# Kernel tuning notes

Hardware: AMD Instinct MI355X
Metric: run time of the kernel (lower is better)

The kernel has to match this reference:

```python
import jax, jax.numpy as jnp
import numpy as np

B, L, DIM = 4, 2048, 1024
EXPAND, D_STATE, D_CONV = 2, 16, 4
D_INNER = EXPAND * DIM          # 2048
DT_RANK = DIM // 16             # 64
MLP_HID = 4 * DIM


def setup_inputs() -> dict:
    key = jax.random.key(0)
    ks = jax.random.split(key, 20)
    s = 0.02
    inp = {
        "hidden_states": jax.random.normal(ks[0], (B, L, DIM), jnp.float32),
        "cond": jax.random.normal(ks[1], (B, DIM), jnp.float32),
        # norm (LayerNorm with affine)
        "norm_w": jnp.ones((DIM,), jnp.float32),
        "norm_b": jnp.zeros((DIM,), jnp.float32),
        # adaLN: Linear(dim, 6*dim)
        "ada_w": jax.random.normal(ks[2], (6 * DIM, DIM), jnp.float32) * s,
        "ada_b": jnp.zeros((6 * DIM,), jnp.float32),
        # Mamba mixer params
        "in_proj_w": jax.random.normal(ks[3], (2 * D_INNER, DIM), jnp.float32) * s,
        "conv_w": jax.random.normal(ks[4], (D_INNER, 1, D_CONV), jnp.float32) * s,
        "conv_b": jnp.zeros((D_INNER,), jnp.float32),
        "x_proj_w": jax.random.normal(ks[5], (DT_RANK + 2 * D_STATE, D_INNER), jnp.float32) * s,
        "dt_proj_w": jax.random.normal(ks[6], (D_INNER, DT_RANK), jnp.float32) * s,
        "dt_proj_b": jax.random.uniform(ks[7], (D_INNER,), jnp.float32, -4.0, -2.0),
        "A_log": jnp.log(jnp.broadcast_to(jnp.arange(1, D_STATE + 1, dtype=jnp.float32), (D_INNER, D_STATE))),
        "Dp": jnp.ones((D_INNER,), jnp.float32),
        "out_proj_w": jax.random.normal(ks[8], (DIM, D_INNER), jnp.float32) * s,
        # MLP
        "fc1_w": jax.random.normal(ks[9], (MLP_HID, DIM), jnp.float32) * s,
        "fc1_b": jnp.zeros((MLP_HID,), jnp.float32),
        "fc2_w": jax.random.normal(ks[10], (DIM, MLP_HID), jnp.float32) * s,
        "fc2_b": jnp.zeros((DIM,), jnp.float32),
    }
    return inp


def _layernorm(x, w, b, eps):
    mu = jnp.mean(x, axis=-1, keepdims=True)
    var = jnp.mean(jnp.square(x - mu), axis=-1, keepdims=True)
    y = (x - mu) * jax.lax.rsqrt(var + eps)
    return y * w + b if w is not None else y


def _modulate(x, shift, scale):
    # x: [B,L,D]; shift/scale: [B,D]
    return x * (1.0 + scale[:, None, :]) + shift[:, None, :]


def _mamba(x_in, in_proj_w, conv_w, conv_b, x_proj_w, dt_proj_w, dt_proj_b, A_log, Dp, out_proj_w):
    # x_in: [B,L,DIM]
    xz = jnp.einsum("bld,ed->ble", x_in, in_proj_w)        # [B,L,2*Di]
    x, z = jnp.split(xz, 2, axis=-1)                        # each [B,L,Di]
    # causal depthwise conv over L
    x_ncl = jnp.transpose(x, (0, 2, 1))                     # [B,Di,L]
    x_ncl = jax.lax.conv_general_dilated(
        x_ncl, conv_w, window_strides=(1,), padding=[(D_CONV - 1, 0)],
        feature_group_count=D_INNER, dimension_numbers=("NCH", "OIH", "NCH"))
    x = jnp.transpose(x_ncl, (0, 2, 1)) + conv_b            # [B,L,Di]
    x = jax.nn.silu(x)
    x_dbl = jnp.einsum("bld,ed->ble", x, x_proj_w)          # [B,L,dt_rank+2*N]
    dt, Bm, Cm = jnp.split(x_dbl, [DT_RANK, DT_RANK + D_STATE], axis=-1)
    dt = jax.nn.softplus(jnp.einsum("blr,dr->bld", dt, dt_proj_w) + dt_proj_b)  # [B,L,Di]
    A = -jnp.exp(A_log)                                     # [Di,N]

    def step(h, inps):
        dt_t, B_t, C_t, x_t = inps                          # [B,Di],[B,N],[B,N],[B,Di]
        dA = jnp.exp(dt_t[..., None] * A)                   # [B,Di,N]
        dBx = (dt_t * x_t)[..., None] * B_t[:, None, :]     # [B,Di,N]
        h = h * dA + dBx
        y = jnp.einsum("bdn,bn->bd", h, C_t)
        return h, y

    h0 = jnp.zeros((x.shape[0], D_INNER, D_STATE), x.dtype)
    xs = (jnp.transpose(dt, (1, 0, 2)), jnp.transpose(Bm, (1, 0, 2)),
          jnp.transpose(Cm, (1, 0, 2)), jnp.transpose(x, (1, 0, 2)))
    _, ys = jax.lax.scan(step, h0, xs)                      # [L,B,Di]
    y = jnp.transpose(ys, (1, 0, 2)) + x * Dp               # [B,L,Di]
    y = y * jax.nn.silu(z)
    return jnp.einsum("bld,od->blo", y, out_proj_w)         # [B,L,DIM]


def reference(hidden_states, cond, norm_w, norm_b, ada_w, ada_b, in_proj_w, conv_w,
              conv_b, x_proj_w, dt_proj_w, dt_proj_b, A_log, Dp, out_proj_w,
              fc1_w, fc1_b, fc2_w, fc2_b):
    residual = hidden_states                                # residual=None path
    hs = _layernorm(residual, norm_w, norm_b, 1e-5)
    mods = jax.nn.silu(cond) @ ada_w.T + ada_b              # [B,6*DIM]
    shift_msa, scale_msa, gate_msa, shift_mlp, scale_mlp, gate_mlp = jnp.split(mods, 6, axis=1)
    hs = gate_msa[:, None, :] * _mamba(_modulate(hs, shift_msa, scale_msa),
                                       in_proj_w, conv_w, conv_b, x_proj_w,
                                       dt_proj_w, dt_proj_b, A_log, Dp, out_proj_w)
    h2 = _modulate(_layernorm(hs, None, None, 1e-6), shift_mlp, scale_mlp)
    h2 = jax.nn.gelu(h2 @ fc1_w.T + fc1_b, approximate=True) @ fc2_w.T + fc2_b
    hs = hs + gate_mlp[:, None, :] * h2
    return (hs, residual)
```

## Files before the change

### kernel.cpp

```cpp
#include <hip/hip_runtime.h>
#include <hip/hip_bf16.h>


typedef unsigned short ushort_t;
typedef __attribute__((ext_vector_type(8))) short short8;
typedef __attribute__((ext_vector_type(4))) float floatx4;
typedef __attribute__((ext_vector_type(4))) unsigned short ushort4v;

#define DEVI __device__ __forceinline__

DEVI float b2f(ushort_t u) { union { unsigned int i; float f; } v; v.i = ((unsigned int)u) << 16; return v.f; }
DEVI ushort_t f2b(float f) {
    union { float f; unsigned int i; } v; v.f = f;
    unsigned int r = v.i + 0x7fffu + ((v.i >> 16) & 1u);
    return (ushort_t)(r >> 16);
}
DEVI bool is_f32(const void* nw) { return ((const unsigned int*)nw)[0] == 0x3F800000u; }
DEVI float sigmoidf_(float x) { return 1.f / (1.f + __expf(-x)); }
DEVI float siluf_(float x) { return x * sigmoidf_(x); }
DEVI float softplusf_(float x) { return (x > 20.f) ? x : log1pf(__expf(x)); }
DEVI float gelu_tanh_(float x) {
    float c = 0.7978845608028654f * (x + 0.044715f * x * x * x);
    return 0.5f * x * (1.f + tanhf(c));
}
DEVI void async16(ushort_t* lds, const ushort_t* g) {
    __builtin_amdgcn_global_load_lds((const __attribute__((address_space(1))) void*)g,
                                     (__attribute__((address_space(3))) void*)lds,
                                     16, 0, 0);
}

DEVI void remap_tile(int bid, int Mt, int Nt, int& mt, int& nt) {
    const int nwg = Mt * Nt;
    const int cpx = nwg >> 3;
    const int v = (bid & 7) * cpx + (bid >> 3);
    if (((Mt & 7) == 0) && ((Nt & 7) == 0)) {
        const int s = v >> 6, w = v & 63;
        const int smt = s % (Mt >> 3), snt = s / (Mt >> 3);
        mt = smt * 8 + (w >> 3);
        nt = snt * 8 + (w & 7);
    } else {
        mt = v % Mt;
        nt = v / Mt;
    }
}

__global__ __launch_bounds__(256) void convert_all_kernel(
    const void* __restrict__ in_proj, const void* __restrict__ x_proj,
    const void* __restrict__ dt_w, const void* __restrict__ out_proj,
    const void* __restrict__ fc1_w, const void* __restrict__ fc2_w,
    const void* __restrict__ dt_b, const void* __restrict__ fc1_b,
    const void* __restrict__ fc2_b,
    ushort_t* __restrict__ w_in, ushort_t* __restrict__ w_xp,
    ushort_t* __restrict__ w_dt, ushort_t* __restrict__ w_out,
    ushort_t* __restrict__ w_fc1, ushort_t* __restrict__ w_fc2,
    float* __restrict__ dtb_f, float* __restrict__ fc1b_f,
    float* __restrict__ fc2b_f, const void* __restrict__ nw)
{
    const bool f32 = is_f32(nw);
    int b = blockIdx.x;
    const void* src; ushort_t* dst; int n8;
    if (b < 2048)      { src = in_proj;  dst = w_in;  n8 = 524288; }
    else if (b < 2144) { src = x_proj;   dst = w_xp;  n8 = 24576;  b -= 2048; }
    else if (b < 2208) { src = dt_w;     dst = w_dt;  n8 = 16384;  b -= 2144; }
    else if (b < 3232) { src = out_proj; dst = w_out; n8 = 262144; b -= 2208; }
    else if (b < 5280) { src = fc1_w;    dst = w_fc1; n8 = 524288; b -= 3232; }
    else if (b < 7328) { src = fc2_w;    dst = w_fc2; n8 = 524288; b -= 5280; }
    else {
        b -= 7328;
        const void* bs; float* bd; int n;
        if (b < 8)       { bs = dt_b;  bd = dtb_f;  n = 2048; }
        else if (b < 24) { bs = fc1_b; bd = fc1b_f; n = 4096; b -= 8; }
        else             { bs = fc2_b; bd = fc2b_f; n = 1024; b -= 24; }
        int i = b * 256 + threadIdx.x;
        if (i < n) bd[i] = f32 ? ((const float*)bs)[i] : b2f(((const ushort_t*)bs)[i]);
        return;
    }
    int i = b * 256 + threadIdx.x;
    if (i >= n8) return;
    if (f32) {
        const float4* s = (const float4*)src;
        float4 a = s[2 * i], c = s[2 * i + 1];
        short8 o;
        o[0] = (short)f2b(a.x); o[1] = (short)f2b(a.y);
        o[2] = (short)f2b(a.z); o[3] = (short)f2b(a.w);
        o[4] = (short)f2b(c.x); o[5] = (short)f2b(c.y);
        o[6] = (short)f2b(c.z); o[7] = (short)f2b(c.w);
        ((short8*)dst)[i] = o;
    } else {
        ((short8*)dst)[i] = ((const short8*)src)[i];
    }
}

__global__ __launch_bounds__(256) void ada_kernel(
    const void* __restrict__ condv, const void* __restrict__ ada_wv,
    const void* __restrict__ ada_bv, float* __restrict__ mods,
    const void* __restrict__ nw)
{
    __shared__ float sc[4096];
    const int tid = threadIdx.x;
    const bool f32 = is_f32(nw);
    if (f32) {
        const float* cf = (const float*)condv;
        for (int i = tid; i < 4096; i += 256) sc[i] = siluf_(cf[i]);
    } else {
        const ushort_t* cb = (const ushort_t*)condv;
        for (int i = tid; i < 4096; i += 256) sc[i] = siluf_(b2f(cb[i]));
    }
    __syncthreads();
    const int j = blockIdx.x * 256 + tid;
    float bb = f32 ? ((const float*)ada_bv)[j] : b2f(((const ushort_t*)ada_bv)[j]);
    float s0 = bb, s1 = bb, s2 = bb, s3 = bb;
    if (f32) {
        const float4* w4 = ((const float4*)ada_wv) + (size_t)j * 256;
        for (int d4 = 0; d4 < 256; d4++) {
            float4 w = w4[d4];
            float wv[4] = {w.x, w.y, w.z, w.w};
#pragma unroll
            for (int e = 0; e < 4; e++) {
                int d = d4 * 4 + e;
                s0 += sc[d] * wv[e];
                s1 += sc[1024 + d] * wv[e];
                s2 += sc[2048 + d] * wv[e];
                s3 += sc[3072 + d] * wv[e];
            }
        }
    } else {
        const ushort_t* wrow = ((const ushort_t*)ada_wv) + (size_t)j * 1024;
        for (int d = 0; d < 1024; d += 8) {
            short8 w8 = *(const short8*)(wrow + d);
#pragma unroll
            for (int e = 0; e < 8; e++) {
                float wv = b2f(((const ushort_t*)&w8)[e]);
                s0 += sc[d + e] * wv;
                s1 += sc[1024 + d + e] * wv;
                s2 += sc[2048 + d + e] * wv;
                s3 += sc[3072 + d + e] * wv;
            }
        }
    }
    mods[0 * 6144 + j] = s0;
    mods[1 * 6144 + j] = s1;
    mods[2 * 6144 + j] = s2;
    mods[3 * 6144 + j] = s3;
}

__global__ __launch_bounds__(256) void ln1_res_kernel(
    const void* __restrict__ hiddenv, const void* __restrict__ nwv,
    const void* __restrict__ nbv, const float* __restrict__ mods,
    ushort_t* __restrict__ xout, void* __restrict__ dout)
{
    const int t = blockIdx.x, tid = threadIdx.x;
    const int bb = t >> 11;
    const bool f32 = is_f32(nwv);
    float vv[4], s = 0.f, ss = 0.f;
    if (f32) {
        float4 u = ((const float4*)((const float*)hiddenv + (size_t)t * 1024))[tid];
        vv[0] = u.x; vv[1] = u.y; vv[2] = u.z; vv[3] = u.w;
        ((float4*)((float*)dout + 8388608))[(size_t)t * 256 + tid] = u;
    } else {
        ushort4v u = ((const ushort4v*)((const ushort_t*)hiddenv + (size_t)t * 1024))[tid];
#pragma unroll
        for (int j = 0; j < 4; j++) vv[j] = b2f(u[j]);
        ((ushort4v*)((ushort_t*)dout + 8388608))[(size_t)t * 256 + tid] = u;
    }
#pragma unroll
    for (int j = 0; j < 4; j++) { s += vv[j]; ss += vv[j] * vv[j]; }
#pragma unroll
    for (int off = 32; off > 0; off >>= 1) { s += __shfl_down(s, off); ss += __shfl_down(ss, off); }
    __shared__ float red[8];
    const int wave = tid >> 6, lane = tid & 63;
    if (lane == 0) { red[wave] = s; red[4 + wave] = ss; }
    __syncthreads();
    s = red[0] + red[1] + red[2] + red[3];
    ss = red[4] + red[5] + red[6] + red[7];
    const float mu = s * (1.f / 1024.f);
    const float var = ss * (1.f / 1024.f) - mu * mu;
    const float rstd = rsqrtf(var + 1e-5f);
    const float* mrow = mods + (size_t)bb * 6144;
    ushort4v o;
#pragma unroll
    for (int j = 0; j < 4; j++) {
        int d = tid * 4 + j;
        float w = f32 ? ((const float*)nwv)[d] : b2f(((const ushort_t*)nwv)[d]);
        float b = f32 ? ((const float*)nbv)[d] : b2f(((const ushort_t*)nbv)[d]);
        float y = (vv[j] - mu) * rstd * w + b;
        y = y * (1.f + mrow[1024 + d]) + mrow[d];
        o[j] = f2b(y);
    }
    ((ushort4v*)(xout + (size_t)t * 1024))[tid] = o;
}

__global__ __launch_bounds__(256) void ln2_mod_kernel(
    const ushort_t* __restrict__ hs, const float* __restrict__ mods,
    ushort_t* __restrict__ xout)
{
    const int t = blockIdx.x, tid = threadIdx.x;
    const int bb = t >> 11;
    ushort4v u = ((const ushort4v*)(hs + (size_t)t * 1024))[tid];
    float vv[4], s = 0.f, ss = 0.f;
#pragma unroll
    for (int j = 0; j < 4; j++) { vv[j] = b2f(u[j]); s += vv[j]; ss += vv[j] * vv[j]; }
#pragma unroll
    for (int off = 32; off > 0; off >>= 1) { s += __shfl_down(s, off); ss += __shfl_down(ss, off); }
    __shared__ float red[8];
    const int wave = tid >> 6, lane = tid & 63;
    if (lane == 0) { red[wave] = s; red[4 + wave] = ss; }
    __syncthreads();
    s = red[0] + red[1] + red[2] + red[3];
    ss = red[4] + red[5] + red[6] + red[7];
    const float mu = s * (1.f / 1024.f);
    const float var = ss * (1.f / 1024.f) - mu * mu;
    const float rstd = rsqrtf(var + 1e-6f);
    const float* mrow = mods + (size_t)bb * 6144;
    ushort4v o;
#pragma unroll
    for (int j = 0; j < 4; j++) {
        int d = tid * 4 + j;
        float y = (vv[j] - mu) * rstd;
        y = y * (1.f + mrow[4096 + d]) + mrow[3072 + d];
        o[j] = f2b(y);
    }
    ((ushort4v*)(xout + (size_t)t * 1024))[tid] = o;
}

__global__ __launch_bounds__(256) void conv_silu_kernel(
    const ushort_t* __restrict__ xb, const void* __restrict__ cwv,
    const void* __restrict__ cbv, ushort_t* __restrict__ xc,
    const void* __restrict__ nw)
{
    const int t = blockIdx.x;
    const int l = t & 2047;
    const int c0 = threadIdx.x * 8;
    const bool f32 = is_f32(nw);
    float acc[8];
    float wlf[32];
    if (f32) {
        const float* cbf = (const float*)cbv;
#pragma unroll
        for (int j = 0; j < 8; j++) acc[j] = cbf[c0 + j];
        const float4* cw4 = (const float4*)((const float*)cwv + (size_t)c0 * 4);
#pragma unroll
        for (int q = 0; q < 8; q++) {
            float4 w = cw4[q];
            wlf[q * 4 + 0] = w.x; wlf[q * 4 + 1] = w.y;
            wlf[q * 4 + 2] = w.z; wlf[q * 4 + 3] = w.w;
        }
    } else {
        const ushort_t* cbb = (const ushort_t*)cbv;
#pragma unroll
        for (int j = 0; j < 8; j++) acc[j] = b2f(cbb[c0 + j]);
        const ushort_t* cwb = (const ushort_t*)cwv + (size_t)c0 * 4;
#pragma unroll
        for (int q = 0; q < 32; q++) wlf[q] = b2f(cwb[q]);
    }
#pragma unroll
    for (int k = 0; k < 4; k++) {
        int tl = l + k - 3;
        if (tl < 0) continue;
        short8 xv = *(const short8*)(xb + (size_t)(t + k - 3) * 2048 + c0);
#pragma unroll
        for (int j = 0; j < 8; j++)
            acc[j] += b2f(((const ushort_t*)&xv)[j]) * wlf[j * 4 + k];
    }
    short8 o;
#pragma unroll
    for (int j = 0; j < 8; j++) ((ushort_t*)&o)[j] = f2b(siluf_(acc[j]));
    *(short8*)(xc + (size_t)t * 2048 + c0) = o;
}

__global__ __launch_bounds__(256) void scan_phase1(
    const ushort_t* __restrict__ dtb, const ushort_t* __restrict__ xcv,
    const ushort_t* __restrict__ xdbl, const void* __restrict__ A_logv,
    ushort_t* __restrict__ Hloc, ushort_t* __restrict__ Pst,
    const void* __restrict__ nw)
{
    const int blk = blockIdx.x;
    const int dblk = blk & 7;
    const int c = (blk >> 3) & 31;
    const int b = blk >> 8;
    const int d = dblk * 256 + threadIdx.x;
    const bool f32 = is_f32(nw);
    float Av[16];
#pragma unroll
    for (int n = 0; n < 16; n++) {
        float al = f32 ? ((const float*)A_logv)[(size_t)d * 16 + n]
                       : b2f(((const ushort_t*)A_logv)[(size_t)d * 16 + n]);
        Av[n] = -__expf(al);
    }
    float h[16], Pa[16];
#pragma unroll
    for (int n = 0; n < 16; n++) { h[n] = 0.f; Pa[n] = 1.f; }
    const int t0 = c * 64;
    size_t tb = ((size_t)b * 2048 + t0) * 2048 + d;
    float dtv = b2f(dtb[tb]);
    float xv  = b2f(xcv[tb]);
    for (int tt = 0; tt < 64; ++tt) {
        float dtn = b2f(dtb[tb + 2048]);
        float xn  = b2f(xcv[tb + 2048]);
        const ushort_t* bp = xdbl + ((size_t)b * 2048 + t0 + tt) * 96 + 64;
        short8 B8a = *(const short8*)bp;
        short8 B8b = *(const short8*)(bp + 8);
        float dtx = dtv * xv;
#pragma unroll
        for (int n = 0; n < 8; n++) {
            float dA = __expf(dtv * Av[n]);
            h[n] = h[n] * dA + dtx * b2f(((const ushort_t*)&B8a)[n]);
            Pa[n] *= dA;
        }
#pragma unroll
        for (int n = 8; n < 16; n++) {
            float dA = __expf(dtv * Av[n]);
            h[n] = h[n] * dA + dtx * b2f(((const ushort_t*)&B8b)[n - 8]);
            Pa[n] *= dA;
        }
        dtv = dtn; xv = xn; tb += 2048;
    }
    const size_t o = (((size_t)c * 4 + b) * 16) * 2048 + d;
#pragma unroll
    for (int n = 0; n < 16; n++) {
        Hloc[o + (size_t)n * 2048] = f2b(h[n]);
        Pst [o + (size_t)n * 2048] = f2b(Pa[n]);
    }
}

__global__ __launch_bounds__(256) void scan_phase2(
    const ushort_t* __restrict__ Hloc, const ushort_t* __restrict__ Pst,
    float* __restrict__ Hin)
{
    const int gi = blockIdx.x * 256 + threadIdx.x;
    const int d = gi & 2047;
    const int n = (gi >> 11) & 15;
    const int b = gi >> 15;
    float h = 0.f;
    const size_t o0 = ((size_t)b * 16 + n) * 2048 + d;
    for (int c = 0; c < 32; ++c) {
        const size_t o = o0 + (size_t)c * (4 * 16 * 2048);
        Hin[o] = h;
        h = b2f(Hloc[o]) + b2f(Pst[o]) * h;
    }
}

__global__ __launch_bounds__(256) void scan_phase3(
    const ushort_t* __restrict__ dtb, ushort_t* __restrict__ xc,
    const ushort_t* __restrict__ xdbl, const ushort_t* __restrict__ zbuf,
    const void* __restrict__ A_logv, const void* __restrict__ Dpv,
    const float* __restrict__ Hin, const void* __restrict__ nw)
{
    const int blk = blockIdx.x;
    const int dblk = blk & 7;
    const int c = (blk >> 3) & 31;
    const int b = blk >> 8;
    const int d = dblk * 256 + threadIdx.x;
    const bool f32 = is_f32(nw);
    float Av[16];
#pragma unroll
    for (int n = 0; n < 16; n++) {
        float al = f32 ? ((const float*)A_logv)[(size_t)d * 16 + n]
                       : b2f(((const ushort_t*)A_logv)[(size_t)d * 16 + n]);
        Av[n] = -__expf(al);
    }
    const float Dv = f32 ? ((const float*)Dpv)[d] : b2f(((const ushort_t*)Dpv)[d]);
    float h[16];
    {
        const size_t o = (((size_t)c * 4 + b) * 16) * 2048 + d;
#pragma unroll
        for (int n = 0; n < 16; n++) h[n] = Hin[o + (size_t)n * 2048];
    }
    const int t0 = c * 64;
    size_t tb = ((size_t)b * 2048 + t0) * 2048 + d;
    float dtv = b2f(dtb[tb]);
    float xv  = b2f(xc[tb]);
    float zv  = b2f(zbuf[tb]);
    for (int tt = 0; tt < 64; ++tt) {
        float dtn = b2f(dtb[tb + 2048]);
        float xn  = b2f(xc[tb + 2048]);
        float zn  = b2f(zbuf[tb + 2048]);
        const ushort_t* bp = xdbl + ((size_t)b * 2048 + t0 + tt) * 96 + 64;
        short8 B8a = *(const short8*)bp;
        short8 B8b = *(const short8*)(bp + 8);
        short8 C8a = *(const short8*)(bp + 16);
        short8 C8b = *(const short8*)(bp + 24);
        float dtx = dtv * xv;
        float y = 0.f;
#pragma unroll
        for (int n = 0; n < 8; n++) {
            float dA = __expf(dtv * Av[n]);
            h[n] = h[n] * dA + dtx * b2f(((const ushort_t*)&B8a)[n]);
            y += h[n] * b2f(((const ushort_t*)&C8a)[n]);
        }
#pragma unroll
        for (int n = 8; n < 16; n++) {
            float dA = __expf(dtv * Av[n]);
            h[n] = h[n] * dA + dtx * b2f(((const ushort_t*)&B8b)[n - 8]);
            y += h[n] * b2f(((const ushort_t*)&C8b)[n - 8]);
        }
        float yo = (y + xv * Dv) * siluf_(zv);
        xc[tb] = f2b(yo);
        dtv = dtn; xv = xn; zv = zn; tb += 2048;
    }
}

template <int EPI>
DEVI void epi_store(int row, int col, float v,
                    void* C0, void* C1, int ldc,
                    const float* bias, const float* mods,
                    const ushort_t* hs, int fl)
{
    if constexpr (EPI == 0) {
        if (col < 2048)
            ((ushort_t*)C0)[(size_t)row * 2048 + col] = f2b(v);
        else
            ((ushort_t*)C1)[(size_t)row * 2048 + (col - 2048)] = f2b(v);
    } else if constexpr (EPI == 1) {
        ((ushort_t*)C0)[(size_t)row * ldc + col] = f2b(v);
    } else if constexpr (EPI == 2) {
        v += bias[col];
        ((ushort_t*)C0)[(size_t)row * ldc + col] = f2b(softplusf_(v));
    } else if constexpr (EPI == 3) {
        const int bb = row >> 11;
        v *= mods[(size_t)bb * 6144 + 2048 + col];
        ((ushort_t*)C0)[(size_t)row * ldc + col] = f2b(v);
    } else if constexpr (EPI == 4) {
        v += bias[col];
        ((ushort_t*)C0)[(size_t)row * ldc + col] = f2b(gelu_tanh_(v));
    } else if constexpr (EPI == 5) {
        v += bias[col];
        const int bb = row >> 11;
        float o = b2f(hs[(size_t)row * 1024 + col]) + mods[(size_t)bb * 6144 + 5120 + col] * v;
        if (fl)
            ((float*)C0)[(size_t)row * ldc + col] = o;
        else
            ((ushort_t*)C0)[(size_t)row * ldc + col] = f2b(o);
    } else if constexpr (EPI == 6) {
        ((float*)C0)[(size_t)row * ldc + col] = v;
    }
}

#define KLOOP_PIPE(NT)                                               \
    stage(0, 0);                                                     \
    {                                                                \
        int cur = 0;                                                 \
        for (int kt = 0; kt < (NT); kt++) {                          \
            if (kt + 1 < (NT)) {                                     \
                stage(cur ^ 1, kt + 1);                              \
                asm volatile("s_waitcnt vmcnt(8)" ::: "memory");     \
            } else {                                                 \
                asm volatile("s_waitcnt vmcnt(0)" ::: "memory");     \
            }                                                        \
            __builtin_amdgcn_sched_barrier(0);                       \
            __builtin_amdgcn_s_barrier();                            \
            __builtin_amdgcn_sched_barrier(0);                       \
            __builtin_amdgcn_s_setprio(1);                           \
            compute(cur);                                            \
            __builtin_amdgcn_s_setprio(0);                           \
            __builtin_amdgcn_sched_barrier(0);                       \
            __builtin_amdgcn_s_barrier();                            \
            __builtin_amdgcn_sched_barrier(0);                       \
            cur ^= 1;                                                \
        }                                                            \
    }

template <int EPI>
__global__ __launch_bounds__(256) void gemm_bt(
    const ushort_t* __restrict__ A, int lda,
    const ushort_t* __restrict__ W, int ldw,
    int M, int N, int K,
    void* __restrict__ C0, void* __restrict__ C1, int ldc,
    const float* __restrict__ bias,
    const float* __restrict__ mods,
    const ushort_t* __restrict__ hs,
    const void* __restrict__ nwp)
{
    __shared__ __align__(16) ushort_t sA[2][128 * 64];
    __shared__ __align__(16) ushort_t sB[2][128 * 64];
    const int tid = threadIdx.x;
    const int wave = tid >> 6, lane = tid & 63;
    int mt, nt;
    if constexpr (EPI == 6) {
        mt = blockIdx.x & 63; nt = 0;
        const int kc = blockIdx.x >> 6;
        A += (size_t)kc * 512;
        W += (size_t)kc * 512;
        C0 = (float*)C0 + (size_t)kc * 8192 * 96;
    } else {
        remap_tile(blockIdx.x, M >> 7, (N + 127) >> 7, mt, nt);
    }
    const int m0 = mt << 7, n0 = nt << 7;
    const int wr = wave >> 1, wc = wave & 1;
    const int r = tid >> 3, c8 = tid & 7;
    const int rs7 = r & 7;
    int fl = 0;
    if constexpr (EPI == 5) fl = is_f32(nwp) ? 1 : 0;

    floatx4 acc[4][4];
#pragma unroll
    for (int m = 0; m < 4; m++)
#pragma unroll
        for (int nn = 0; nn < 4; nn++) acc[m][nn] = floatx4{0.f, 0.f, 0.f, 0.f};

    auto stage = [&](int buf, int kt) {
        const int kb = kt << 6;
#pragma unroll
        for (int i = 0; i < 4; i++) {
            const int row = i * 32 + r;
            async16(&sA[buf][(size_t)row * 64 + c8 * 8],
                    A + (size_t)(m0 + row) * lda + kb + ((c8 ^ rs7) << 3));
            int rB = n0 + row; if (rB >= N) rB = N - 1;
            async16(&sB[buf][(size_t)row * 64 + c8 * 8],
                    W + (size_t)rB * ldw + kb + ((c8 ^ rs7) << 3));
        }
    };
    auto compute = [&](int buf) {
#pragma unroll
        for (int kk = 0; kk < 2; kk++) {
            const int sw = ((kk * 4 + (lane >> 4)) ^ (lane & 7)) << 3;
            short8 bfr[4];
#pragma unroll
            for (int nn = 0; nn < 4; nn++)
                bfr[nn] = *(const short8*)&sB[buf][(size_t)(wc * 64 + nn * 16 + (lane & 15)) * 64 + sw];
#pragma unroll
            for (int m = 0; m < 4; m++) {
                short8 af = *(const short8*)&sA[buf][(size_t)(wr * 64 + m * 16 + (lane & 15)) * 64 + sw];
#pragma unroll
                for (int nn = 0; nn < 4; nn++)
                    acc[m][nn] = __builtin_amdgcn_mfma_f32_16x16x32_bf16(af, bfr[nn], acc[m][nn], 0, 0, 0);
            }
        }
    };

    const int NT = K >> 6;
    KLOOP_PIPE(NT)

    const int erow = wr * 64 + ((lane >> 4) << 2);
    const int ecol = wc * 64 + (lane & 15);
#pragma unroll
    for (int m = 0; m < 4; m++)
#pragma unroll
        for (int nn = 0; nn < 4; nn++) {
            const int col = n0 + ecol + nn * 16;
            if (col >= N) continue;
#pragma unroll
            for (int rr = 0; rr < 4; rr++)
                epi_store<EPI>(m0 + erow + m * 16 + rr, col, acc[m][nn][rr],
                               C0, C1, ldc, bias, mods, hs, fl);
        }
}

template <int EPI>
__global__ __launch_bounds__(512) void gemm256(
    const ushort_t* __restrict__ A, int lda,
    const ushort_t* __restrict__ W, int ldw,
    int M, int N, int K,
    void* __restrict__ C0, void* __restrict__ C1, int ldc,
    const float* __restrict__ bias,
    const float* __restrict__ mods,
    const ushort_t* __restrict__ hs,
    const void* __restrict__ nwp)
{
    __shared__ __align__(16) ushort_t sA[2][4][256 * 16];
    __shared__ __align__(16) ushort_t sB[2][4][256 * 16];
    const int tid = threadIdx.x;
    const int wave = tid >> 6, lane = tid & 63;
    const int l15 = lane & 15, j8 = lane >> 4;
    int mt, nt;
    remap_tile(blockIdx.x, M >> 8, N >> 8, mt, nt);
    const int m0 = mt << 8, n0 = nt << 8;
    const int wr = wave >> 2, wc = wave & 3;
    const int srow = tid >> 1, scs = tid & 1;
    const int ssrc = scs ^ ((srow >> 2) & 1);
    int fl = 0;
    if constexpr (EPI == 5) fl = is_f32(nwp) ? 1 : 0;

    floatx4 acc[8][4];
#pragma unroll
    for (int m = 0; m < 8; m++)
#pragma unroll
        for (int nn = 0; nn < 4; nn++) acc[m][nn] = floatx4{0.f, 0.f, 0.f, 0.f};

    auto stage = [&](int buf, int kt, int p) {
        const int kb = (kt << 6) + (p << 4);
        async16(&sA[buf][p][srow * 16 + scs * 8],
                A + (size_t)(m0 + srow) * lda + kb + ssrc * 8);
        async16(&sB[buf][p][srow * 16 + scs * 8],
                W + (size_t)(n0 + srow) * ldw + kb + ssrc * 8);
    };

    short8 afA[4], bfA[4], afB[4], bfB[4];

#define RD256(AF, BF, BUF, KK, MLO)                                             \
    {                                                                           \
        const int sl_ = (KK) * 2 + (j8 >> 1);                                   \
        const int h_ = j8 & 1;                                                  \
        _Pragma("unroll")                                                       \
        for (int nn = 0; nn < 4; nn++) {                                        \
            const int row_ = wc * 64 + nn * 16 + l15;                           \
            BF[nn] = *(const short8*)&sB[BUF][sl_]                              \
                         [row_ * 16 + ((h_ ^ ((row_ >> 2) & 1)) << 3)];         \
        }                                                                       \
        _Pragma("unroll")                                                       \
        for (int i = 0; i < 4; i++) {                                           \
            const int row_ = wr * 128 + ((MLO) + i) * 16 + l15;                 \
            AF[i] = *(const short8*)&sA[BUF][sl_]                               \
                        [row_ * 16 + ((h_ ^ ((row_ >> 2) & 1)) << 3)];          \
        }                                                                       \
    }

#define MM256(AF, BF, MLO)                                                      \
    {                                                                           \
        __builtin_amdgcn_s_setprio(1);                                          \
        _Pragma("unroll")                                                       \
        for (int i = 0; i < 4; i++)                                             \
            _Pragma("unroll")                                                   \
            for (int nn = 0; nn < 4; nn++)                                      \
                acc[(MLO) + i][nn] = __builtin_amdgcn_mfma_f32_16x16x32_bf16(   \
                    AF[i], BF[nn], acc[(MLO) + i][nn], 0, 0, 0);                \
        __builtin_amdgcn_s_setprio(0);                                          \
    }

#define SBAR256                                                                 \
    __builtin_amdgcn_sched_barrier(0);                                          \
    __builtin_amdgcn_s_barrier();                                               \
    __builtin_amdgcn_sched_barrier(0);

    const int NT = K >> 6;
#pragma unroll
    for (int p = 0; p < 4; p++) stage(0, 0, p);
    asm volatile("s_waitcnt vmcnt(4)" ::: "memory");
    SBAR256
    RD256(afA, bfA, 0, 0, 0)
    int cur = 0;
    for (int kt = 0; kt < NT; kt++) {
        const bool pre = (kt + 1 < NT);
        if (pre) stage(cur ^ 1, kt + 1, 0);
        RD256(afB, bfB, cur, 0, 4)
        MM256(afA, bfA, 0)
        if (pre) { asm volatile("s_waitcnt vmcnt(2)" ::: "memory"); }
        else     { asm volatile("s_waitcnt vmcnt(0)" ::: "memory"); }
        SBAR256
        if (pre) stage(cur ^ 1, kt + 1, 1);
        RD256(afA, bfA, cur, 1, 0)
        MM256(afB, bfB, 4)
        SBAR256
        if (pre) stage(cur ^ 1, kt + 1, 2);
        RD256(afB, bfB, cur, 1, 4)
        MM256(afA, bfA, 0)
        if (pre) { asm volatile("s_waitcnt vmcnt(2)" ::: "memory"); }
        SBAR256
        if (pre) {
            stage(cur ^ 1, kt + 1, 3);
            RD256(afA, bfA, cur ^ 1, 0, 0)
        }
        MM256(afB, bfB, 4)
        SBAR256
        cur ^= 1;
    }
#undef RD256
#undef MM256
#undef SBAR256

    const int erow = wr * 128 + (j8 << 2);
    const int ecol = wc * 64 + l15;
#pragma unroll
    for (int m = 0; m < 8; m++)
#pragma unroll
        for (int nn = 0; nn < 4; nn++) {
            const int col = n0 + ecol + nn * 16;
            if (col >= N) continue;
#pragma unroll
            for (int rr = 0; rr < 4; rr++)
                epi_store<EPI>(m0 + erow + m * 16 + rr, col, acc[m][nn][rr],
                               C0, C1, ldc, bias, mods, hs, fl);
        }
}

__global__ __launch_bounds__(256) void xp_reduce_kernel(
    const float* __restrict__ part, ushort_t* __restrict__ x_dbl)
{
    const int i = blockIdx.x * 256 + threadIdx.x;
    float s = part[i] + part[i + 786432] + part[i + 2 * 786432] + part[i + 3 * 786432];
    x_dbl[i] = f2b(s);
}

extern "C" void kernel_launch(void* const* d_in, const int* in_sizes, int n_in,
                              void* d_out, int out_size, void* d_ws, size_t ws_size,
                              hipStream_t stream)
{
    const void* hidden   = d_in[0];
    const void* cond     = d_in[1];
    const void* norm_w   = d_in[2];
    const void* norm_b   = d_in[3];
    const void* ada_w    = d_in[4];
    const void* ada_b    = d_in[5];
    const void* in_proj  = d_in[6];
    const void* conv_w   = d_in[7];
    const void* conv_b   = d_in[8];
    const void* x_proj   = d_in[9];
    const void* dt_w     = d_in[10];
    const void* dt_b     = d_in[11];
    const void* A_log    = d_in[12];
    const void* Dp       = d_in[13];
    const void* out_proj = d_in[14];
    const void* fc1_w    = d_in[15];
    const void* fc1_b    = d_in[16];
    const void* fc2_w    = d_in[17];
    const void* fc2_b    = d_in[18];

    constexpr size_t OFF_MODS  = 256;
    constexpr size_t OFF_DTB_F = 131072;
    constexpr size_t OFF_FC1B  = 139264;
    constexpr size_t OFF_FC2B  = 155648;
    constexpr size_t OFF_WIN   = 262144;
    constexpr size_t OFF_WXP   = 8650752;
    constexpr size_t OFF_WDT   = 9043968;
    constexpr size_t OFF_WOUT  = 9306112;
    constexpr size_t OFF_WFC1  = 13500416;
    constexpr size_t OFF_WFC2  = 21889024;
    constexpr size_t OFF_XBUF  = 30277632;
    constexpr size_t OFF_ZBUF  = 63832064;
    constexpr size_t OFF_XCONV = 97386496;
    constexpr size_t OFF_XIN   = 130940928;
    constexpr size_t OFF_XDBL  = 147718144;
    constexpr size_t OFF_HS    = 149291008;
    constexpr size_t WS_NEED   = 166068224;
    if (ws_size < WS_NEED) return;

    char* ws = (char*)d_ws;
    float*    mods   = (float*)(ws + OFF_MODS);
    float*    dtb_f  = (float*)(ws + OFF_DTB_F);
    float*    fc1b_f = (float*)(ws + OFF_FC1B);
    float*    fc2b_f = (float*)(ws + OFF_FC2B);
    ushort_t* w_in   = (ushort_t*)(ws + OFF_WIN);
    ushort_t* w_xp   = (ushort_t*)(ws + OFF_WXP);
    ushort_t* w_dt   = (ushort_t*)(ws + OFF_WDT);
    ushort_t* w_out  = (ushort_t*)(ws + OFF_WOUT);
    ushort_t* w_fc1  = (ushort_t*)(ws + OFF_WFC1);
    ushort_t* w_fc2  = (ushort_t*)(ws + OFF_WFC2);
    ushort_t* xbuf   = (ushort_t*)(ws + OFF_XBUF);
    ushort_t* zbuf   = (ushort_t*)(ws + OFF_ZBUF);
    ushort_t* x_conv = (ushort_t*)(ws + OFF_XCONV);
    ushort_t* x_in   = (ushort_t*)(ws + OFF_XIN);
    ushort_t* x_dbl  = (ushort_t*)(ws + OFF_XDBL);
    ushort_t* hsb    = (ushort_t*)(ws + OFF_HS);
    ushort_t* dtb    = xbuf;
    ushort_t* h1     = xbuf;
    ushort_t* h2in   = x_in;
    float*    xp_part= (float*)(ws + OFF_XIN);
    ushort_t* Hloc   = (ushort_t*)(ws + OFF_XIN);
    ushort_t* Pst    = (ushort_t*)(ws + OFF_XIN + 8388608);
    float*    Hin    = (float*)(ws + OFF_HS);

    convert_all_kernel<<<7356, 256, 0, stream>>>(
        in_proj, x_proj, dt_w, out_proj, fc1_w, fc2_w, dt_b, fc1_b, fc2_b,
        w_in, w_xp, w_dt, w_out, w_fc1, w_fc2, dtb_f, fc1b_f, fc2b_f, norm_w);

    ada_kernel<<<24, 256, 0, stream>>>(cond, ada_w, ada_b, mods, norm_w);
    ln1_res_kernel<<<8192, 256, 0, stream>>>(hidden, norm_w, norm_b, mods, x_in, d_out);
    gemm256<0><<<512, 512, 0, stream>>>(x_in, 1024, w_in, 1024, 8192, 4096, 1024,
                                        xbuf, zbuf, 2048, nullptr, nullptr, nullptr, nullptr);
    conv_silu_kernel<<<8192, 256, 0, stream>>>(xbuf, conv_w, conv_b, x_conv, norm_w);
    gemm_bt<6><<<256, 256, 0, stream>>>(x_conv, 2048, w_xp, 2048, 8192, 96, 512,
                                        xp_part, nullptr, 96, nullptr, nullptr, nullptr, nullptr);
    xp_reduce_kernel<<<3072, 256, 0, stream>>>(xp_part, x_dbl);
    gemm_bt<2><<<1024, 256, 0, stream>>>(x_dbl, 96, w_dt, 64, 8192, 2048, 64,
                                         dtb, nullptr, 2048, dtb_f, nullptr, nullptr, nullptr);
    scan_phase1<<<1024, 256, 0, stream>>>(dtb, x_conv, x_dbl, A_log, Hloc, Pst, norm_w);
    scan_phase2<<<512, 256, 0, stream>>>(Hloc, Pst, Hin);
    scan_phase3<<<1024, 256, 0, stream>>>(dtb, x_conv, x_dbl, zbuf, A_log, Dp, Hin, norm_w);
    gemm_bt<3><<<512, 256, 0, stream>>>(x_conv, 2048, w_out, 2048, 8192, 1024, 2048,
                                        hsb, nullptr, 1024, nullptr, mods, nullptr, nullptr);
    ln2_mod_kernel<<<8192, 256, 0, stream>>>(hsb, mods, h2in);
    gemm256<4><<<512, 512, 0, stream>>>(h2in, 1024, w_fc1, 1024, 8192, 4096, 1024,
                                        h1, nullptr, 4096, fc1b_f, nullptr, nullptr, nullptr);
    gemm_bt<5><<<512, 256, 0, stream>>>(h1, 4096, w_fc2, 4096, 8192, 1024, 4096,
                                        d_out, nullptr, 1024, fc2b_f, mods, hsb, norm_w);
}
```

Measured before the change: 766.5 us.

## Split 256-tile GEMM into two-phase and front-loaded eight-phase pipeline variants

Adds a gemm256_2ph kernel for the in_proj GEMM. It uses a flat 256x64 XOR-swizzled shared tile, a simple stage/compute double buffer driven by KLOOP_PIPE, and plain unpipelined fragment reads. The fc1 GEMM keeps the 8-phase ping-pong kernel, but all four k-slices of the next tile are now issued at the start of each iteration instead of one per phase, with the vmcnt waits adjusted to match. The aim is to expose more outstanding global loads earlier and to test a simpler schedule for in_proj, at the cost of losing fine-grained interleaving of loads with MFMA phases.

```diff
diff --git a/kernel.cpp b/kernel.cpp
--- a/kernel.cpp
+++ b/kernel.cpp
@@ -547,7 +547,84 @@
 }
 
 template <int EPI>
-__global__ __launch_bounds__(512) void gemm256(
+__global__ __launch_bounds__(512) void gemm256_2ph(
+    const ushort_t* __restrict__ A, int lda,
+    const ushort_t* __restrict__ W, int ldw,
+    int M, int N, int K,
+    void* __restrict__ C0, void* __restrict__ C1, int ldc,
+    const float* __restrict__ bias,
+    const float* __restrict__ mods,
+    const ushort_t* __restrict__ hs,
+    const void* __restrict__ nwp)
+{
+    __shared__ __align__(16) ushort_t sA[2][256 * 64];
+    __shared__ __align__(16) ushort_t sB[2][256 * 64];
+    const int tid = threadIdx.x;
+    const int wave = tid >> 6, lane = tid & 63;
+    int mt, nt;
+    remap_tile(blockIdx.x, M >> 8, N >> 8, mt, nt);
+    const int m0 = mt << 8, n0 = nt << 8;
+    const int wr = wave >> 2, wc = wave & 3;
+    const int r = tid >> 3, c8 = tid & 7;
+    const int rs7 = r & 7;
+    int fl = 0;
+    if constexpr (EPI == 5) fl = is_f32(nwp) ? 1 : 0;
+
+    floatx4 acc[8][4];
+#pragma unroll
+    for (int m = 0; m < 8; m++)
+#pragma unroll
+        for (int nn = 0; nn < 4; nn++) acc[m][nn] = floatx4{0.f, 0.f, 0.f, 0.f};
+
+    auto stage = [&](int buf, int kt) {
+        const int kb = kt << 6;
+#pragma unroll
+        for (int i = 0; i < 4; i++) {
+            const int row = i * 64 + r;
+            async16(&sA[buf][(size_t)row * 64 + c8 * 8],
+                    A + (size_t)(m0 + row) * lda + kb + ((c8 ^ rs7) << 3));
+            async16(&sB[buf][(size_t)row * 64 + c8 * 8],
+                    W + (size_t)(n0 + row) * ldw + kb + ((c8 ^ rs7) << 3));
+        }
+    };
+    auto compute = [&](int buf) {
+#pragma unroll
+        for (int kk = 0; kk < 2; kk++) {
+            const int sw = ((kk * 4 + (lane >> 4)) ^ (lane & 7)) << 3;
+            short8 bfr[4];
+#pragma unroll
+            for (int nn = 0; nn < 4; nn++)
+                bfr[nn] = *(const short8*)&sB[buf][(size_t)(wc * 64 + nn * 16 + (lane & 15)) * 64 + sw];
+#pragma unroll
+            for (int m = 0; m < 8; m++) {
+                short8 af = *(const short8*)&sA[buf][(size_t)(wr * 128 + m * 16 + (lane & 15)) * 64 + sw];
+#pragma unroll
+                for (int nn = 0; nn < 4; nn++)
+                    acc[m][nn] = __builtin_amdgcn_mfma_f32_16x16x32_bf16(af, bfr[nn], acc[m][nn], 0, 0, 0);
+            }
+        }
+    };
+
+    const int NT = K >> 6;
+    KLOOP_PIPE(NT)
+
+    const int erow = wr * 128 + ((lane >> 4) << 2);
+    const int ecol = wc * 64 + (lane & 15);
+#pragma unroll
+    for (int m = 0; m < 8; m++)
+#pragma unroll
+        for (int nn = 0; nn < 4; nn++) {
+            const int col = n0 + ecol + nn * 16;
+            if (col >= N) continue;
+#pragma unroll
+            for (int rr = 0; rr < 4; rr++)
+                epi_store<EPI>(m0 + erow + m * 16 + rr, col, acc[m][nn][rr],
+                               C0, C1, ldc, bias, mods, hs, fl);
+        }
+}
+
+template <int EPI>
+__global__ __launch_bounds__(512) void gemm256_8ph(
     const ushort_t* __restrict__ A, int lda,
     const ushort_t* __restrict__ W, int ldw,
     int M, int N, int K,
@@ -577,12 +654,15 @@
 #pragma unroll
         for (int nn = 0; nn < 4; nn++) acc[m][nn] = floatx4{0.f, 0.f, 0.f, 0.f};
 
-    auto stage = [&](int buf, int kt, int p) {
-        const int kb = (kt << 6) + (p << 4);
-        async16(&sA[buf][p][srow * 16 + scs * 8],
-                A + (size_t)(m0 + srow) * lda + kb + ssrc * 8);
-        async16(&sB[buf][p][srow * 16 + scs * 8],
-                W + (size_t)(n0 + srow) * ldw + kb + ssrc * 8);
+    auto stage4 = [&](int buf, int kt) {
+#pragma unroll
+        for (int p = 0; p < 4; p++) {
+            const int kb = (kt << 6) + (p << 4);
+            async16(&sA[buf][p][srow * 16 + scs * 8],
+                    A + (size_t)(m0 + srow) * lda + kb + ssrc * 8);
+            async16(&sB[buf][p][srow * 16 + scs * 8],
+                    W + (size_t)(n0 + srow) * ldw + kb + ssrc * 8);
+        }
     };
 
     short8 afA[4], bfA[4], afB[4], bfB[4];
@@ -623,33 +703,27 @@
     __builtin_amdgcn_sched_barrier(0);
 
     const int NT = K >> 6;
-#pragma unroll
-    for (int p = 0; p < 4; p++) stage(0, 0, p);
+    stage4(0, 0);
     asm volatile("s_waitcnt vmcnt(4)" ::: "memory");
     SBAR256
     RD256(afA, bfA, 0, 0, 0)
     int cur = 0;
     for (int kt = 0; kt < NT; kt++) {
         const bool pre = (kt + 1 < NT);
-        if (pre) stage(cur ^ 1, kt + 1, 0);
+        if (pre) stage4(cur ^ 1, kt + 1);
         RD256(afB, bfB, cur, 0, 4)
         MM256(afA, bfA, 0)
-        if (pre) { asm volatile("s_waitcnt vmcnt(2)" ::: "memory"); }
+        if (pre) { asm volatile("s_waitcnt vmcnt(8)" ::: "memory"); }
         else     { asm volatile("s_waitcnt vmcnt(0)" ::: "memory"); }
         SBAR256
-        if (pre) stage(cur ^ 1, kt + 1, 1);
         RD256(afA, bfA, cur, 1, 0)
         MM256(afB, bfB, 4)
         SBAR256
-        if (pre) stage(cur ^ 1, kt + 1, 2);
         RD256(afB, bfB, cur, 1, 4)
         MM256(afA, bfA, 0)
-        if (pre) { asm volatile("s_waitcnt vmcnt(2)" ::: "memory"); }
+        if (pre) { asm volatile("s_waitcnt vmcnt(4)" ::: "memory"); }
         SBAR256
-        if (pre) {
-            stage(cur ^ 1, kt + 1, 3);
-            RD256(afA, bfA, cur ^ 1, 0, 0)
-        }
+        if (pre) { RD256(afA, bfA, cur ^ 1, 0, 0) }
         MM256(afB, bfB, 4)
         SBAR256
         cur ^= 1;
@@ -755,8 +829,8 @@
 
     ada_kernel<<<24, 256, 0, stream>>>(cond, ada_w, ada_b, mods, norm_w);
     ln1_res_kernel<<<8192, 256, 0, stream>>>(hidden, norm_w, norm_b, mods, x_in, d_out);
-    gemm256<0><<<512, 512, 0, stream>>>(x_in, 1024, w_in, 1024, 8192, 4096, 1024,
-                                        xbuf, zbuf, 2048, nullptr, nullptr, nullptr, nullptr);
+    gemm256_2ph<0><<<512, 512, 0, stream>>>(x_in, 1024, w_in, 1024, 8192, 4096, 1024,
+                                            xbuf, zbuf, 2048, nullptr, nullptr, nullptr, nullptr);
     conv_silu_kernel<<<8192, 256, 0, stream>>>(xbuf, conv_w, conv_b, x_conv, norm_w);
     gemm_bt<6><<<256, 256, 0, stream>>>(x_conv, 2048, w_xp, 2048, 8192, 96, 512,
                                         xp_part, nullptr, 96, nullptr, nullptr, nullptr, nullptr);
@@ -769,8 +843,8 @@
     gemm_bt<3><<<512, 256, 0, stream>>>(x_conv, 2048, w_out, 2048, 8192, 1024, 2048,
                                         hsb, nullptr, 1024, nullptr, mods, nullptr, nullptr);
     ln2_mod_kernel<<<8192, 256, 0, stream>>>(hsb, mods, h2in);
-    gemm256<4><<<512, 512, 0, stream>>>(h2in, 1024, w_fc1, 1024, 8192, 4096, 1024,
-                                        h1, nullptr, 4096, fc1b_f, nullptr, nullptr, nullptr);
+    gemm256_8ph<4><<<512, 512, 0, stream>>>(h2in, 1024, w_fc1, 1024, 8192, 4096, 1024,
+                                            h1, nullptr, 4096, fc1b_f, nullptr, nullptr, nullptr);
     gemm_bt<5><<<512, 256, 0, stream>>>(h1, 4096, w_fc2, 4096, 8192, 1024, 4096,
                                         d_out, nullptr, 1024, fc2b_f, mods, hsb, norm_w);
 }
```

Result: faster. 737.5 us (-3.8%).
